# Kernel optimization log

Hardware: AMD Instinct MI355X
Metric: run time of the kernel (lower is better)

The kernel has to match this reference:

```python
import jax, jax.numpy as jnp
import numpy as np

N, E, D_IN, HID, H, L = 20000, 320000, 64, 128, 4, 3
D_HEAD = HID  # PyG TransformerConv: out_channels is the per-head dim
LN_EPS = 1e-5


def setup_inputs() -> dict:
    key = jax.random.key(0)
    ks = jax.random.split(key, 12)
    x = jax.random.normal(ks[0], (N, D_IN), dtype=jnp.float32)
    edge_index = jax.random.randint(ks[1], (2, E), 0, N, dtype=jnp.int64)
    s_in = 1.0 / np.sqrt(D_IN)
    s_h = 1.0 / np.sqrt(HID)
    Win = jax.random.normal(ks[2], (D_IN, HID), dtype=jnp.float32) * s_in
    bin_ = jnp.zeros((HID,), dtype=jnp.float32)
    Wq = jax.random.normal(ks[3], (L, HID, H * D_HEAD), dtype=jnp.float32) * s_h
    Wk = jax.random.normal(ks[4], (L, HID, H * D_HEAD), dtype=jnp.float32) * s_h
    Wv = jax.random.normal(ks[5], (L, HID, H * D_HEAD), dtype=jnp.float32) * s_h
    bq = jnp.zeros((L, H * D_HEAD), dtype=jnp.float32)
    bk = jnp.zeros((L, H * D_HEAD), dtype=jnp.float32)
    bv = jnp.zeros((L, H * D_HEAD), dtype=jnp.float32)
    Wskip = jax.random.normal(ks[6], (L, HID, HID), dtype=jnp.float32) * s_h
    bskip = jnp.zeros((L, HID), dtype=jnp.float32)
    ln_gamma = jnp.ones((L, HID), dtype=jnp.float32)
    ln_beta = jnp.zeros((L, HID), dtype=jnp.float32)
    return dict(x=x, edge_index=edge_index, Win=Win, bin_=bin_, Wq=Wq, bq=bq,
                Wk=Wk, bk=bk, Wv=Wv, bv=bv, Wskip=Wskip, bskip=bskip,
                ln_gamma=ln_gamma, ln_beta=ln_beta)


def _segment_softmax(logits, seg, num_segments):
    # logits: [E, H], seg: [E] destination node ids
    m = jax.ops.segment_max(logits, seg, num_segments=num_segments)  # [N, H]
    ex = jnp.exp(logits - m[seg])
    s = jax.ops.segment_sum(ex, seg, num_segments=num_segments)  # [N, H]
    return ex / (s[seg] + 1e-16)


def _layer_norm(x, gamma, beta):
    mu = jnp.mean(x, axis=-1, keepdims=True)
    var = jnp.mean(jnp.square(x - mu), axis=-1, keepdims=True)
    return (x - mu) * jax.lax.rsqrt(var + LN_EPS) * gamma + beta


def _transformer_conv(h, src, dst, Wq, bq, Wk, bk, Wv, bv, Wskip, bskip):
    q = (h @ Wq + bq).reshape(N, H, D_HEAD)
    k = (h @ Wk + bk).reshape(N, H, D_HEAD)
    v = (h @ Wv + bv).reshape(N, H, D_HEAD)
    scale = 1.0 / np.sqrt(D_HEAD)
    logits = jnp.einsum('ehd,ehd->eh', q[dst], k[src]) * scale  # [E, H]
    alpha = _segment_softmax(logits, dst, N)  # [E, H]
    msg = alpha[:, :, None] * v[src]  # [E, H, D_HEAD]
    out = jax.ops.segment_sum(msg, dst, num_segments=N)  # [N, H, D_HEAD]
    out = out.mean(axis=1)  # concat=False -> mean over heads
    return out + h @ Wskip + bskip  # root_weight skip (lin_skip)


def reference(x, edge_index, Win, bin_, Wq, bq, Wk, bk, Wv, bv, Wskip, bskip, ln_gamma, ln_beta):
    src = edge_index[0]
    dst = edge_index[1]
    h = x @ Win + bin_
    for l in range(L):
        h_new = _transformer_conv(h, src, dst, Wq[l], bq[l], Wk[l], bk[l],
                                  Wv[l], bv[l], Wskip[l], bskip[l])
        h = _layer_norm(h + h_new, ln_gamma[l], ln_beta[l])
    return h
```

## Files before the change

### kernel.cpp

```cpp
#include <hip/hip_runtime.h>
#include <hip/hip_bf16.h>
#include <math.h>

#define NN 20000
#define EE 320000
#define DIN 64
#define HIDC 128
#define NCOLS 1664
#define NL 3

typedef __attribute__((ext_vector_type(8))) short bf16x8;
typedef __attribute__((ext_vector_type(8))) unsigned short u16x8;
typedef __attribute__((ext_vector_type(4))) float f32x4;

__device__ __forceinline__ float bf2f(unsigned short u) {
  union { unsigned i; float f; } v; v.i = ((unsigned)u) << 16; return v.f;
}
__device__ __forceinline__ unsigned short f2bf(float f) {
  __hip_bfloat16 b = __float2bfloat16(f);
  return *(unsigned short*)&b;
}

__device__ __forceinline__ unsigned char f2fp8(float f) {
#if __has_builtin(__builtin_amdgcn_cvt_pk_fp8_f32)
  return (unsigned char)(__builtin_amdgcn_cvt_pk_fp8_f32(f, f, 0, 0) & 0xFF);
#else
  unsigned b = __float_as_uint(f);
  unsigned s = (b >> 24) & 0x80u;
  float a = fabsf(f);
  if (a < 0.015625f) return (unsigned char)s;
  unsigned mag = __float_as_uint(fminf(a, 448.f));
  mag += 0x7FFFFu + ((mag >> 20) & 1u);
  unsigned code = (mag >> 20) - (120u << 3);
  if (code > 0x7Eu) code = 0x7Eu;
  return (unsigned char)(s | code);
#endif
}

__device__ __forceinline__ float fp82f(unsigned b) {
  unsigned x = ((b & 0x80u) << 24) | ((b & 0x7fu) << 20);
  return __uint_as_float(x) * 0x1p+120f;
}

__device__ __forceinline__ void dec8(uint2 u, float* f) {
#if __has_builtin(__builtin_amdgcn_cvt_pk_f32_fp8)
  {
    auto p0 = __builtin_amdgcn_cvt_pk_f32_fp8(u.x, 0);
    auto p1 = __builtin_amdgcn_cvt_pk_f32_fp8(u.x, 1);
    auto p2 = __builtin_amdgcn_cvt_pk_f32_fp8(u.y, 0);
    auto p3 = __builtin_amdgcn_cvt_pk_f32_fp8(u.y, 1);
    f[0] = p0[0]; f[1] = p0[1]; f[2] = p1[0]; f[3] = p1[1];
    f[4] = p2[0]; f[5] = p2[1]; f[6] = p3[0]; f[7] = p3[1];
  }
#else
#pragma unroll
  for (int i = 0; i < 4; i++) f[i] = fp82f((u.x >> (8 * i)) & 0xFFu);
#pragma unroll
  for (int i = 0; i < 4; i++) f[4 + i] = fp82f((u.y >> (8 * i)) & 0xFFu);
#endif
}

__global__ void build_wcatT_all(const float* __restrict__ Wq, const float* __restrict__ Wk,
                                const float* __restrict__ Wv, const float* __restrict__ Wsk,
                                unsigned short* __restrict__ wT) {
  int idx = blockIdx.x * 256 + threadIdx.x;
  if (idx >= NL * NCOLS * HIDC) return;
  int l = idx / (NCOLS * HIDC);
  int rem = idx - l * (NCOLS * HIDC);
  int n = rem >> 7, k = rem & 127;
  float v;
  if (n < 512)       v = Wq[(size_t)l * HIDC * 512 + (size_t)k * 512 + n];
  else if (n < 1024) v = Wk[(size_t)l * HIDC * 512 + (size_t)k * 512 + (n - 512)];
  else if (n < 1536) v = Wv[(size_t)l * HIDC * 512 + (size_t)k * 512 + (n - 1024)];
  else               v = Wsk[(size_t)l * HIDC * HIDC + (size_t)k * 128 + (n - 1536)];
  wT[idx] = f2bf(v);
}

__global__ void build_bcat_all(const float* __restrict__ bq, const float* __restrict__ bk,
                               const float* __restrict__ bv, const float* __restrict__ bsk,
                               float* __restrict__ bcat) {
  int idx = blockIdx.x * 256 + threadIdx.x;
  if (idx >= NL * NCOLS) return;
  int l = idx / NCOLS, m = idx - l * NCOLS;
  float v;
  if (m < 512)       v = bq[l * 512 + m];
  else if (m < 1024) v = bk[l * 512 + (m - 512)];
  else if (m < 1536) v = bv[l * 512 + (m - 1024)];
  else               v = bsk[l * 128 + (m - 1536)];
  bcat[idx] = v;
}

__global__ void build_winT(const float* __restrict__ Win, unsigned short* __restrict__ winT) {
  int idx = blockIdx.x * 256 + threadIdx.x;
  if (idx >= HIDC * DIN) return;
  int c = idx >> 6, k = idx & 63;
  winT[idx] = f2bf(Win[(size_t)k * HIDC + c]);
}

__global__ void conv_x(const float* __restrict__ x, unsigned short* __restrict__ xb) {
  int i = blockIdx.x * 256 + threadIdx.x;
  if (i * 4 >= NN * DIN) return;
  float4 v = *(const float4*)(x + (size_t)i * 4);
  ushort4 o = make_ushort4(f2bf(v.x), f2bf(v.y), f2bf(v.z), f2bf(v.w));
  *(ushort4*)(xb + (size_t)i * 4) = o;
}

__global__ void deg_hist(const int* __restrict__ ei, int* __restrict__ deg) {
  int e = blockIdx.x * 256 + threadIdx.x;
  if (e >= EE) return;
  atomicAdd(&deg[ei[EE + e]], 1);
}

__global__ __launch_bounds__(1024) void scan_deg(const int* __restrict__ deg,
                                                 int* __restrict__ rowstart) {
  __shared__ int part[1024];
  int t = threadIdx.x;
  int base = t * 20;
  int local[20];
  int s = 0;
#pragma unroll
  for (int i = 0; i < 20; i++) {
    int idx = base + i;
    int d = (idx < NN) ? deg[idx] : 0;
    local[i] = d;
    s += d;
  }
  part[t] = s;
  __syncthreads();
  for (int d = 1; d < 1024; d <<= 1) {
    int v = (t >= d) ? part[t - d] : 0;
    __syncthreads();
    part[t] += v;
    __syncthreads();
  }
  int run = part[t] - s;
#pragma unroll
  for (int i = 0; i < 20; i++) {
    int idx = base + i;
    if (idx < NN) rowstart[idx] = run;
    run += local[i];
  }
  if (t == 1023) rowstart[NN] = part[1023];
}

__global__ void csr_scatter(const int* __restrict__ ei, const int* __restrict__ rowstart,
                            int* __restrict__ cur, int* __restrict__ csrc) {
  int e = blockIdx.x * 256 + threadIdx.x;
  if (e >= EE) return;
  int src = ei[e], dst = ei[EE + e];
  int pos = atomicAdd(&cur[dst], 1);
  csrc[rowstart[dst] + pos] = src;
}

__device__ __forceinline__ void gl_lds16(const void* g, void* l) {
  __builtin_amdgcn_global_load_lds((const unsigned int*)g, (unsigned int*)l, 16, 0, 0);
}

template <int K>
__device__ __forceinline__ void stage_tile(const unsigned short* gbase,
                                           unsigned char* lbase, int tid) {
  constexpr int CH = K / 8;
  constexpr int ISS = (128 * CH) / 256;
  int wave = tid >> 6;
#pragma unroll
  for (int p = 0; p < ISS; p++) {
    int slot = p * 256 + tid;
    int row = slot / CH, ch = slot % CH;
    const unsigned short* src = gbase + (size_t)row * K + ((ch ^ (row & 7)) * 8);
    unsigned char* ldst = lbase + (size_t)(p * 256 + wave * 64) * 16;
    gl_lds16(src, ldst);
  }
}

template <int K>
__device__ __forceinline__ bf16x8 read_frag(const unsigned char* lbase, int row, int kk, int lk) {
  int ch = (kk * 4 + lk) ^ (row & 7);
  return *(const bf16x8*)(lbase + (size_t)row * (K * 2) + ch * 16);
}

__global__ __launch_bounds__(256) void mfma_gemm_in(
    const unsigned short* __restrict__ A, const unsigned short* __restrict__ BT,
    const float* __restrict__ bias, unsigned short* __restrict__ outb,
    float* __restrict__ outf) {
  __shared__ __align__(16) unsigned char LDS[34816];
  const int tid = threadIdx.x;
  const int lane = tid & 63, wave = tid >> 6;
  const int lm = lane & 15, lk = lane >> 4;
  const int wm = wave >> 1, wn = wave & 1;
  const int row0 = blockIdx.x * 128, col0 = 0;
  unsigned char* aL = LDS;
  unsigned char* bL = LDS + 128 * 64 * 2;

  stage_tile<64>(A + (size_t)row0 * 64, aL, tid);
  stage_tile<64>(BT + (size_t)col0 * 64, bL, tid);
  __syncthreads();

  f32x4 acc[4][4] = {};
  bf16x8 af[4][2];
#pragma unroll
  for (int mf = 0; mf < 4; mf++)
#pragma unroll
    for (int kk = 0; kk < 2; kk++)
      af[mf][kk] = read_frag<64>(aL, wm * 64 + mf * 16 + lm, kk, lk);
#pragma unroll
  for (int nf = 0; nf < 4; nf++) {
    bf16x8 bf[2];
#pragma unroll
    for (int kk = 0; kk < 2; kk++)
      bf[kk] = read_frag<64>(bL, wn * 64 + nf * 16 + lm, kk, lk);
#pragma unroll
    for (int mf = 0; mf < 4; mf++)
#pragma unroll
      for (int kk = 0; kk < 2; kk++)
        acc[mf][nf] = __builtin_amdgcn_mfma_f32_16x16x32_bf16(af[mf][kk], bf[kk],
                                                              acc[mf][nf], 0, 0, 0);
  }
  __syncthreads();

  unsigned short* bb = (unsigned short*)LDS;
#pragma unroll
  for (int nf = 0; nf < 4; nf++) {
    int c = wn * 64 + nf * 16 + lm;
    float bv = bias[c];
#pragma unroll
    for (int mf = 0; mf < 4; mf++)
#pragma unroll
      for (int i = 0; i < 4; i++) {
        int row = wm * 64 + mf * 16 + lk * 4 + i;
        float o = acc[mf][nf][i] + bv;
        bb[row * 136 + c] = f2bf(o);
        int r = row0 + row;
        if (r < NN) outf[(size_t)r * HIDC + c] = o;
      }
  }
  __syncthreads();
#pragma unroll
  for (int p = 0; p < 8; p++) {
    int idx = p * 256 + tid;
    int row = idx >> 4, c = idx & 15;
    int gr = row0 + row;
    if (gr < NN) {
      uint4 v = *(const uint4*)(bb + row * 136 + c * 8);
      *(uint4*)(outb + (size_t)gr * HIDC + c * 8) = v;
    }
  }
}

__global__ __launch_bounds__(256, 5) void gemm64(
    const unsigned short* __restrict__ A, const unsigned short* __restrict__ BT,
    const float* __restrict__ bias, unsigned short* __restrict__ qb,
    unsigned char* __restrict__ kv8, float* __restrict__ skipb,
    int nbx, int nwg) {
  __shared__ __align__(16) unsigned char LDS[32768];
  const int tid = threadIdx.x;
  int orig = blockIdx.x;
  int qq = nwg >> 3, rr8 = nwg & 7;
  int xcd = orig & 7, slot = orig >> 3;
  int wg = (xcd < rr8 ? xcd * (qq + 1) : rr8 * (qq + 1) + (xcd - rr8) * qq) + slot;
  const int bx = wg % nbx, by = wg / nbx;

  const int lane = tid & 63, wave = tid >> 6;
  const int lm = lane & 15, lk = lane >> 4;
  const int wm = wave >> 1, wn = wave & 1;
  const int row0 = by * 64, col0 = bx * 64;
  unsigned char* aL = LDS;
  unsigned char* bL = LDS + 16384;

  {
    const unsigned short* gA = A + (size_t)row0 * 128;
    const unsigned short* gB = BT + (size_t)col0 * 128;
#pragma unroll
    for (int p = 0; p < 4; p++) {
      int sl = p * 256 + tid;
      int row = sl >> 4, ch = sl & 15;
      gl_lds16(gA + (size_t)row * 128 + ((ch ^ (row & 7)) * 8),
               aL + (size_t)(p * 256 + wave * 64) * 16);
    }
#pragma unroll
    for (int p = 0; p < 4; p++) {
      int sl = p * 256 + tid;
      int row = sl >> 4, ch = sl & 15;
      gl_lds16(gB + (size_t)row * 128 + ((ch ^ (row & 7)) * 8),
               bL + (size_t)(p * 256 + wave * 64) * 16);
    }
  }
  __syncthreads();

  f32x4 acc[2][2] = {};
  bf16x8 af[2][4], bf[2][4];
#pragma unroll
  for (int mf = 0; mf < 2; mf++)
#pragma unroll
    for (int kk = 0; kk < 4; kk++)
      af[mf][kk] = read_frag<128>(aL, wm * 32 + mf * 16 + lm, kk, lk);
#pragma unroll
  for (int nf = 0; nf < 2; nf++)
#pragma unroll
    for (int kk = 0; kk < 4; kk++)
      bf[nf][kk] = read_frag<128>(bL, wn * 32 + nf * 16 + lm, kk, lk);
#pragma unroll
  for (int nf = 0; nf < 2; nf++)
#pragma unroll
    for (int mf = 0; mf < 2; mf++)
#pragma unroll
      for (int kk = 0; kk < 4; kk++)
        acc[mf][nf] = __builtin_amdgcn_mfma_f32_16x16x32_bf16(af[mf][kk], bf[nf][kk],
                                                              acc[mf][nf], 0, 0, 0);
  __syncthreads();

  if (bx >= 24) {
    const int cbase = col0 - 1536;
#pragma unroll
    for (int nf = 0; nf < 2; nf++) {
      int c = wn * 32 + nf * 16 + lm;
      float bv = bias[col0 + c];
#pragma unroll
      for (int mf = 0; mf < 2; mf++)
#pragma unroll
        for (int i = 0; i < 4; i++) {
          int r = row0 + wm * 32 + mf * 16 + lk * 4 + i;
          if (r < NN) skipb[(size_t)r * HIDC + cbase + c] = acc[mf][nf][i] + bv;
        }
    }
  } else if (bx >= 8) {
    unsigned char* bb8 = LDS;
#pragma unroll
    for (int nf = 0; nf < 2; nf++) {
      int c = wn * 32 + nf * 16 + lm;
      float bv = bias[col0 + c];
#pragma unroll
      for (int mf = 0; mf < 2; mf++)
#pragma unroll
        for (int i = 0; i < 4; i++) {
          int row = wm * 32 + mf * 16 + lk * 4 + i;
          bb8[row * 80 + c] = f2fp8(acc[mf][nf][i] + bv);
        }
    }
    __syncthreads();
    const int kvcol0 = col0 - 512;
    {
      int row = tid >> 2, cw = tid & 3;
      int gr = row0 + row;
      if (gr < NN) {
        uint4 v = *(const uint4*)(bb8 + row * 80 + cw * 16);
        *(uint4*)(kv8 + (size_t)gr * 1024 + kvcol0 + cw * 16) = v;
      }
    }
  } else {
    unsigned short* bb = (unsigned short*)LDS;
#pragma unroll
    for (int nf = 0; nf < 2; nf++) {
      int c = wn * 32 + nf * 16 + lm;
      float bv = bias[col0 + c];
#pragma unroll
      for (int mf = 0; mf < 2; mf++)
#pragma unroll
        for (int i = 0; i < 4; i++) {
          int row = wm * 32 + mf * 16 + lk * 4 + i;
          bb[row * 80 + c] = f2bf(acc[mf][nf][i] + bv);
        }
    }
    __syncthreads();
#pragma unroll
    for (int p = 0; p < 2; p++) {
      int idx = p * 256 + tid;
      int row = idx >> 3, cw = idx & 7;
      int gr = row0 + row;
      if (gr < NN) {
        uint4 v = *(const uint4*)(bb + row * 80 + cw * 8);
        *(uint4*)(qb + (size_t)gr * 512 + col0 + cw * 8) = v;
      }
    }
  }
}

__global__ __launch_bounds__(256) void node_fused(
    const unsigned short* __restrict__ qb, const unsigned char* __restrict__ kv8,
    const float* __restrict__ skipb,
    const float* __restrict__ h, const int* __restrict__ rowstart,
    const int* __restrict__ csrc,
    const float* __restrict__ gamma, const float* __restrict__ beta,
    float* __restrict__ outp, unsigned short* __restrict__ hb_out) {
  int n = blockIdx.x * 4 + (threadIdx.x >> 6);
  if (n >= NN) return;
  int lane = threadIdx.x & 63;
  int hh = lane >> 4, t = lane & 15;
  int j0 = rowstart[n], j1 = rowstart[n + 1];

  u16x8 q8 = *(const u16x8*)(qb + (size_t)n * 512 + hh * 128 + t * 8);
  float qf[8];
#pragma unroll
  for (int i = 0; i < 8; i++) qf[i] = bf2f(q8[i]);

  const unsigned char* kb = kv8 + hh * 128 + t * 8;
  const unsigned char* vb = kv8 + 512 + hh * 128 + t * 8;

  float m = -INFINITY, s = 0.f;
  float acc[8] = {0.f, 0.f, 0.f, 0.f, 0.f, 0.f, 0.f, 0.f};

  int j = j0;
  for (; j + 3 < j1; j += 4) {
    int s4[4];
#pragma unroll
    for (int e = 0; e < 4; e++) s4[e] = csrc[j + e];
    uint2 kk4[4], vv4[4];
#pragma unroll
    for (int e = 0; e < 4; e++) {
      kk4[e] = *(const uint2*)(kb + (size_t)s4[e] * 1024);
      vv4[e] = *(const uint2*)(vb + (size_t)s4[e] * 1024);
    }
    float lg4[4];
#pragma unroll
    for (int e = 0; e < 4; e++) {
      float kf[8];
      dec8(kk4[e], kf);
      float p = 0.f;
#pragma unroll
      for (int i = 0; i < 8; i++) p += qf[i] * kf[i];
      p += __shfl_xor(p, 1);
      p += __shfl_xor(p, 2);
      p += __shfl_xor(p, 4);
      p += __shfl_xor(p, 8);
      lg4[e] = p * 0.08838834764831845f;
    }
    float mx = fmaxf(fmaxf(lg4[0], lg4[1]), fmaxf(lg4[2], lg4[3]));
    if (mx > m) {
      float rr = __expf(m - mx);
      s *= rr;
#pragma unroll
      for (int i = 0; i < 8; i++) acc[i] *= rr;
      m = mx;
    }
#pragma unroll
    for (int e = 0; e < 4; e++) {
      float w = __expf(lg4[e] - m);
      s += w;
      float vf[8];
      dec8(vv4[e], vf);
#pragma unroll
      for (int i = 0; i < 8; i++) acc[i] += w * vf[i];
    }
  }
  for (; j < j1; ++j) {
    int sA = csrc[j];
    uint2 kA = *(const uint2*)(kb + (size_t)sA * 1024);
    uint2 vA = *(const uint2*)(vb + (size_t)sA * 1024);
    float kfA[8], vfA[8];
    dec8(kA, kfA); dec8(vA, vfA);
    float pA = 0.f;
#pragma unroll
    for (int i = 0; i < 8; i++) pA += qf[i] * kfA[i];
    pA += __shfl_xor(pA, 1);
    pA += __shfl_xor(pA, 2);
    pA += __shfl_xor(pA, 4);
    pA += __shfl_xor(pA, 8);
    float lgA = pA * 0.08838834764831845f;
    if (lgA > m) {
      float rr = __expf(m - lgA);
      s *= rr;
#pragma unroll
      for (int i = 0; i < 8; i++) acc[i] *= rr;
      m = lgA;
    }
    float wA = __expf(lgA - m);
    s += wA;
#pragma unroll
    for (int i = 0; i < 8; i++) acc[i] += wA * vfA[i];
  }

  float rsel = 0.25f / (s + 1e-16f);
#pragma unroll
  for (int i = 0; i < 8; i++) {
    float a = acc[i] * rsel;
    a += __shfl_xor(a, 16);
    a += __shfl_xor(a, 32);
    acc[i] = a;
  }

  size_t hbase = (size_t)n * HIDC;
  float u[8];
  {
    float4 h0 = *(const float4*)(h + hbase + t * 8);
    float4 h1 = *(const float4*)(h + hbase + t * 8 + 4);
    float4 k0 = *(const float4*)(skipb + hbase + t * 8);
    float4 k1 = *(const float4*)(skipb + hbase + t * 8 + 4);
    u[0] = h0.x + acc[0] + k0.x; u[1] = h0.y + acc[1] + k0.y;
    u[2] = h0.z + acc[2] + k0.z; u[3] = h0.w + acc[3] + k0.w;
    u[4] = h1.x + acc[4] + k1.x; u[5] = h1.y + acc[5] + k1.y;
    u[6] = h1.z + acc[6] + k1.z; u[7] = h1.w + acc[7] + k1.w;
  }
  float su = 0.f;
#pragma unroll
  for (int i = 0; i < 8; i++) su += u[i];
#pragma unroll
  for (int d = 1; d < 16; d <<= 1) su += __shfl_xor(su, d);
  float mu = su * (1.f / 128.f);
  float vs = 0.f;
#pragma unroll
  for (int i = 0; i < 8; i++) { u[i] -= mu; vs += u[i] * u[i]; }
#pragma unroll
  for (int d = 1; d < 16; d <<= 1) vs += __shfl_xor(vs, d);
  float inv = rsqrtf(vs * (1.f / 128.f) + 1e-5f);
  if (hh == 0) {
    float4 g0 = *(const float4*)(gamma + t * 8);
    float4 g1 = *(const float4*)(gamma + t * 8 + 4);
    float4 b0 = *(const float4*)(beta + t * 8);
    float4 b1 = *(const float4*)(beta + t * 8 + 4);
    float o[8];
    o[0] = u[0] * inv * g0.x + b0.x; o[1] = u[1] * inv * g0.y + b0.y;
    o[2] = u[2] * inv * g0.z + b0.z; o[3] = u[3] * inv * g0.w + b0.w;
    o[4] = u[4] * inv * g1.x + b1.x; o[5] = u[5] * inv * g1.y + b1.y;
    o[6] = u[6] * inv * g1.z + b1.z; o[7] = u[7] * inv * g1.w + b1.w;
    *(float4*)(outp + hbase + t * 8)     = make_float4(o[0], o[1], o[2], o[3]);
    *(float4*)(outp + hbase + t * 8 + 4) = make_float4(o[4], o[5], o[6], o[7]);
    ushort4 c0 = make_ushort4(f2bf(o[0]), f2bf(o[1]), f2bf(o[2]), f2bf(o[3]));
    ushort4 c1 = make_ushort4(f2bf(o[4]), f2bf(o[5]), f2bf(o[6]), f2bf(o[7]));
    *(ushort4*)(hb_out + hbase + t * 8)     = c0;
    *(ushort4*)(hb_out + hbase + t * 8 + 4) = c1;
  }
}

#define OFF_H      ((size_t)0)
#define OFF_SKIP   ((size_t)2560000)
#define OFF_QB     ((size_t)5120000)
#define OFF_KV8    ((size_t)10240000)
#define OFF_HB     ((size_t)15360000)
#define OFF_XB     ((size_t)16640000)
#define OFF_WT     ((size_t)17280000)
#define OFF_WINT   ((size_t)17599488)
#define OFF_BCAT   ((size_t)17603584)
#define OFF_CSRC   ((size_t)17608576)
#define OFF_ROW    ((size_t)17928576)
#define OFF_DEG    ((size_t)17948580)
#define OFF_CUR    ((size_t)17968580)

extern "C" void kernel_launch(void* const* d_in, const int* in_sizes, int n_in,
                              void* d_out, int out_size, void* d_ws, size_t ws_size,
                              hipStream_t stream) {
  const float* x    = (const float*)d_in[0];
  const int*   ei   = (const int*)d_in[1];
  const float* Win  = (const float*)d_in[2];
  const float* bin_ = (const float*)d_in[3];
  const float* Wq   = (const float*)d_in[4];
  const float* bq   = (const float*)d_in[5];
  const float* Wk   = (const float*)d_in[6];
  const float* bk   = (const float*)d_in[7];
  const float* Wv   = (const float*)d_in[8];
  const float* bv   = (const float*)d_in[9];
  const float* Wsk  = (const float*)d_in[10];
  const float* bsk  = (const float*)d_in[11];
  const float* lng  = (const float*)d_in[12];
  const float* lnb  = (const float*)d_in[13];
  float* out = (float*)d_out;
  float* ws = (float*)d_ws;

  float* h     = ws + OFF_H;
  float* skipb = ws + OFF_SKIP;
  unsigned short* qb   = (unsigned short*)(ws + OFF_QB);
  unsigned char*  kv8  = (unsigned char*)(ws + OFF_KV8);
  unsigned short* hb   = (unsigned short*)(ws + OFF_HB);
  unsigned short* xb   = (unsigned short*)(ws + OFF_XB);
  unsigned short* wT   = (unsigned short*)(ws + OFF_WT);
  unsigned short* winT = (unsigned short*)(ws + OFF_WINT);
  float* bcat  = ws + OFF_BCAT;
  int* csrc     = (int*)(ws + OFF_CSRC);
  int* rowstart = (int*)(ws + OFF_ROW);
  int* deg      = (int*)(ws + OFF_DEG);
  int* cur      = (int*)(ws + OFF_CUR);

  hipMemsetAsync(deg, 0, NN * sizeof(int), stream);
  hipMemsetAsync(cur, 0, NN * sizeof(int), stream);
  deg_hist<<<(EE + 255) / 256, 256, 0, stream>>>(ei, deg);
  scan_deg<<<1, 1024, 0, stream>>>(deg, rowstart);
  csr_scatter<<<(EE + 255) / 256, 256, 0, stream>>>(ei, rowstart, cur, csrc);

  conv_x<<<(NN * DIN / 4 + 255) / 256, 256, 0, stream>>>(x, xb);
  build_winT<<<(HIDC * DIN + 255) / 256, 256, 0, stream>>>(Win, winT);
  build_wcatT_all<<<(NL * NCOLS * HIDC + 255) / 256, 256, 0, stream>>>(
      Wq, Wk, Wv, Wsk, wT);
  build_bcat_all<<<(NL * NCOLS + 255) / 256, 256, 0, stream>>>(bq, bk, bv, bsk, bcat);

  mfma_gemm_in<<<(NN + 127) / 128, 256, 0, stream>>>(xb, winT, bin_, hb, h);

  const int nbx = NCOLS / 64;
  const int nby = (NN + 63) / 64;
  const int nwg = nbx * nby;

  for (int l = 0; l < NL; ++l) {
    gemm64<<<nwg, 256, 0, stream>>>(hb, wT + (size_t)l * NCOLS * HIDC,
                                    bcat + (size_t)l * NCOLS, qb, kv8, skipb,
                                    nbx, nwg);

    float* dst = (l == NL - 1) ? out : h;
    node_fused<<<(NN + 3) / 4, 256, 0, stream>>>(
        qb, kv8, skipb, h, rowstart, csrc,
        lng + (size_t)l * 128, lnb + (size_t)l * 128, dst, hb);
  }
  (void)in_sizes; (void)n_in; (void)out_size; (void)ws_size;
}
```

Before: 312.9 us.

## Interleave FP8 K and V per lane for single 16-byte gathers

The K/V projection GEMM now loads weight rows so that each 64-column tile holds matching K and V slices, and writes them interleaved so every lane's 8 K bytes and 8 V bytes sit next to each other. The edge loop then does one 16-byte gather per neighbor instead of two 8-byte gathers. CSR source ids are stored pre-shifted by the row stride to save address math, and the softmax uses exp2 with the log2(e) factor folded into the logit scale. This changes the kv8 layout, so the GEMM epilogue and the gather kernel must stay consistent.

```diff
diff --git a/kernel.cpp b/kernel.cpp
--- a/kernel.cpp
+++ b/kernel.cpp
@@ -8,6 +8,7 @@
 #define HIDC 128
 #define NCOLS 1664
 #define NL 3
+#define LG2SCALE 0.12751659601518297f
 
 typedef __attribute__((ext_vector_type(8))) short bf16x8;
 typedef __attribute__((ext_vector_type(8))) unsigned short u16x8;
@@ -149,7 +150,7 @@
   if (e >= EE) return;
   int src = ei[e], dst = ei[EE + e];
   int pos = atomicAdd(&cur[dst], 1);
-  csrc[rowstart[dst] + pos] = src;
+  csrc[rowstart[dst] + pos] = src << 10;
 }
 
 __device__ __forceinline__ void gl_lds16(const void* g, void* l) {
@@ -187,12 +188,12 @@
   const int lane = tid & 63, wave = tid >> 6;
   const int lm = lane & 15, lk = lane >> 4;
   const int wm = wave >> 1, wn = wave & 1;
-  const int row0 = blockIdx.x * 128, col0 = 0;
+  const int row0 = blockIdx.x * 128;
   unsigned char* aL = LDS;
   unsigned char* bL = LDS + 128 * 64 * 2;
 
   stage_tile<64>(A + (size_t)row0 * 64, aL, tid);
-  stage_tile<64>(BT + (size_t)col0 * 64, bL, tid);
+  stage_tile<64>(BT, bL, tid);
   __syncthreads();
 
   f32x4 acc[4][4] = {};
@@ -263,12 +264,12 @@
   const int lm = lane & 15, lk = lane >> 4;
   const int wm = wave >> 1, wn = wave & 1;
   const int row0 = by * 64, col0 = bx * 64;
+  const int kvbase = (bx - 8) * 32;
   unsigned char* aL = LDS;
   unsigned char* bL = LDS + 16384;
 
   {
     const unsigned short* gA = A + (size_t)row0 * 128;
-    const unsigned short* gB = BT + (size_t)col0 * 128;
 #pragma unroll
     for (int p = 0; p < 4; p++) {
       int sl = p * 256 + tid;
@@ -276,12 +277,24 @@
       gl_lds16(gA + (size_t)row * 128 + ((ch ^ (row & 7)) * 8),
                aL + (size_t)(p * 256 + wave * 64) * 16);
     }
-#pragma unroll
-    for (int p = 0; p < 4; p++) {
-      int sl = p * 256 + tid;
-      int row = sl >> 4, ch = sl & 15;
-      gl_lds16(gB + (size_t)row * 128 + ((ch ^ (row & 7)) * 8),
-               bL + (size_t)(p * 256 + wave * 64) * 16);
+    if (bx >= 8 && bx < 24) {
+#pragma unroll
+      for (int p = 0; p < 4; p++) {
+        int sl = p * 256 + tid;
+        int row = sl >> 4, ch = sl & 15;
+        int grow = (row < 32) ? (512 + kvbase + row) : (1024 + kvbase + row - 32);
+        gl_lds16(BT + (size_t)grow * 128 + ((ch ^ (row & 7)) * 8),
+                 bL + (size_t)(p * 256 + wave * 64) * 16);
+      }
+    } else {
+      const unsigned short* gB = BT + (size_t)col0 * 128;
+#pragma unroll
+      for (int p = 0; p < 4; p++) {
+        int sl = p * 256 + tid;
+        int row = sl >> 4, ch = sl & 15;
+        gl_lds16(gB + (size_t)row * 128 + ((ch ^ (row & 7)) * 8),
+                 bL + (size_t)(p * 256 + wave * 64) * 16);
+      }
     }
   }
   __syncthreads();
@@ -327,23 +340,24 @@
 #pragma unroll
     for (int nf = 0; nf < 2; nf++) {
       int c = wn * 32 + nf * 16 + lm;
-      float bv = bias[col0 + c];
+      int jj = c & 31;
+      float bv = bias[(c < 32) ? (512 + kvbase + jj) : (1024 + kvbase + jj)];
+      int lc = ((jj >> 3) << 4) + ((c < 32) ? 0 : 8) + (jj & 7);
 #pragma unroll
       for (int mf = 0; mf < 2; mf++)
 #pragma unroll
         for (int i = 0; i < 4; i++) {
           int row = wm * 32 + mf * 16 + lk * 4 + i;
-          bb8[row * 80 + c] = f2fp8(acc[mf][nf][i] + bv);
+          bb8[row * 80 + lc] = f2fp8(acc[mf][nf][i] + bv);
         }
     }
     __syncthreads();
-    const int kvcol0 = col0 - 512;
     {
       int row = tid >> 2, cw = tid & 3;
       int gr = row0 + row;
       if (gr < NN) {
         uint4 v = *(const uint4*)(bb8 + row * 80 + cw * 16);
-        *(uint4*)(kv8 + (size_t)gr * 1024 + kvcol0 + cw * 16) = v;
+        *(uint4*)(kv8 + (size_t)gr * 1024 + 2 * kvbase + cw * 16) = v;
       }
     }
   } else {
@@ -392,8 +406,7 @@
 #pragma unroll
   for (int i = 0; i < 8; i++) qf[i] = bf2f(q8[i]);
 
-  const unsigned char* kb = kv8 + hh * 128 + t * 8;
-  const unsigned char* vb = kv8 + 512 + hh * 128 + t * 8;
+  const unsigned char* kvp = kv8 + hh * 256 + t * 16;
 
   float m = -INFINITY, s = 0.f;
   float acc[8] = {0.f, 0.f, 0.f, 0.f, 0.f, 0.f, 0.f, 0.f};
@@ -403,17 +416,14 @@
     int s4[4];
 #pragma unroll
     for (int e = 0; e < 4; e++) s4[e] = csrc[j + e];
-    uint2 kk4[4], vv4[4];
-#pragma unroll
-    for (int e = 0; e < 4; e++) {
-      kk4[e] = *(const uint2*)(kb + (size_t)s4[e] * 1024);
-      vv4[e] = *(const uint2*)(vb + (size_t)s4[e] * 1024);
-    }
+    uint4 kv4[4];
+#pragma unroll
+    for (int e = 0; e < 4; e++) kv4[e] = *(const uint4*)(kvp + (size_t)s4[e]);
     float lg4[4];
 #pragma unroll
     for (int e = 0; e < 4; e++) {
       float kf[8];
-      dec8(kk4[e], kf);
+      dec8(make_uint2(kv4[e].x, kv4[e].y), kf);
       float p = 0.f;
 #pragma unroll
       for (int i = 0; i < 8; i++) p += qf[i] * kf[i];
@@ -421,11 +431,11 @@
       p += __shfl_xor(p, 2);
       p += __shfl_xor(p, 4);
       p += __shfl_xor(p, 8);
-      lg4[e] = p * 0.08838834764831845f;
+      lg4[e] = p * LG2SCALE;
     }
     float mx = fmaxf(fmaxf(lg4[0], lg4[1]), fmaxf(lg4[2], lg4[3]));
     if (mx > m) {
-      float rr = __expf(m - mx);
+      float rr = exp2f(m - mx);
       s *= rr;
 #pragma unroll
       for (int i = 0; i < 8; i++) acc[i] *= rr;
@@ -433,20 +443,19 @@
     }
 #pragma unroll
     for (int e = 0; e < 4; e++) {
-      float w = __expf(lg4[e] - m);
+      float w = exp2f(lg4[e] - m);
       s += w;
       float vf[8];
-      dec8(vv4[e], vf);
+      dec8(make_uint2(kv4[e].z, kv4[e].w), vf);
 #pragma unroll
       for (int i = 0; i < 8; i++) acc[i] += w * vf[i];
     }
   }
   for (; j < j1; ++j) {
-    int sA = csrc[j];
-    uint2 kA = *(const uint2*)(kb + (size_t)sA * 1024);
-    uint2 vA = *(const uint2*)(vb + (size_t)sA * 1024);
+    uint4 kv = *(const uint4*)(kvp + (size_t)csrc[j]);
     float kfA[8], vfA[8];
-    dec8(kA, kfA); dec8(vA, vfA);
+    dec8(make_uint2(kv.x, kv.y), kfA);
+    dec8(make_uint2(kv.z, kv.w), vfA);
     float pA = 0.f;
 #pragma unroll
     for (int i = 0; i < 8; i++) pA += qf[i] * kfA[i];
@@ -454,15 +463,15 @@
     pA += __shfl_xor(pA, 2);
     pA += __shfl_xor(pA, 4);
     pA += __shfl_xor(pA, 8);
-    float lgA = pA * 0.08838834764831845f;
+    float lgA = pA * LG2SCALE;
     if (lgA > m) {
-      float rr = __expf(m - lgA);
+      float rr = exp2f(m - lgA);
       s *= rr;
 #pragma unroll
       for (int i = 0; i < 8; i++) acc[i] *= rr;
       m = lgA;
     }
-    float wA = __expf(lgA - m);
+    float wA = exp2f(lgA - m);
     s += wA;
 #pragma unroll
     for (int i = 0; i < 8; i++) acc[i] += wA * vfA[i];
```

New measurement: 312.7 us. No clear change (-0.1%).
